# Kernel optimization log

Measured on AMD Instinct MI355X. Metric: run time of the kernel, lower is better.

## Reference

```python
import jax, jax.numpy as jnp
import numpy as np

# Canonical Mamba hyperparams (mamba_ssm defaults for d_model=128)
D_MODEL = 128
D_INNER = 2 * D_MODEL          # expand = 2
D_STATE = 16
D_CONV = 4
DT_RANK = (D_MODEL + 15) // 16  # ceil(d_model/16) = 8
B, N, T = 16, 256, 64
EPS = 1e-5


def setup_inputs() -> dict:
    key = jax.random.key(0)
    ks = jax.random.split(key, 10)
    sc = 0.02
    x = jax.random.normal(ks[0], (B, N, D_MODEL, T), jnp.float32)
    gamma = jnp.ones((D_MODEL,), jnp.float32)
    beta = jnp.zeros((D_MODEL,), jnp.float32)
    W_in = jax.random.normal(ks[1], (D_MODEL, 2 * D_INNER), jnp.float32) * sc
    conv_w = jax.random.normal(ks[2], (D_INNER, D_CONV), jnp.float32) * sc
    conv_b = jnp.zeros((D_INNER,), jnp.float32)
    W_x = jax.random.normal(ks[3], (D_INNER, DT_RANK + 2 * D_STATE), jnp.float32) * sc
    W_dt = jax.random.normal(ks[4], (DT_RANK, D_INNER), jnp.float32) * sc
    b_dt = jax.random.normal(ks[5], (D_INNER,), jnp.float32) * sc
    # S4D-real init: A_log = log(1..d_state), broadcast over channels
    A_log = jnp.log(jnp.broadcast_to(
        jnp.arange(1, D_STATE + 1, dtype=jnp.float32), (D_INNER, D_STATE)))
    Dskip = jnp.ones((D_INNER,), jnp.float32)
    W_out = jax.random.normal(ks[6], (D_INNER, D_MODEL), jnp.float32) * sc
    return dict(x=x, gamma=gamma, beta=beta, W_in=W_in, conv_w=conv_w,
                conv_b=conv_b, W_x=W_x, W_dt=W_dt, b_dt=b_dt,
                A_log=A_log, Dskip=Dskip, W_out=W_out)


def _forward(x, gamma, beta, W_in, conv_w, conv_b, W_x, W_dt, b_dt,
             A_log, Dskip, W_out):
    Bb, Nn, Fd, Tt = x.shape
    # (B,N,F,T) -> (B*N, T, F)
    x_in = x.transpose(0, 1, 3, 2).reshape(Bb * Nn, Tt, Fd)

    # LayerNorm over feature dim
    mu = x_in.mean(-1, keepdims=True)
    var = jnp.mean((x_in - mu) ** 2, axis=-1, keepdims=True)
    u = (x_in - mu) * jax.lax.rsqrt(var + EPS) * gamma + beta

    # Mamba: input projection -> (x, z)
    xz = u @ W_in                                   # (BN,T,2*dI)
    xc, z = jnp.split(xz, 2, axis=-1)

    # Depthwise causal conv1d over time (kernel D_CONV) + SiLU
    xp = jnp.pad(xc, ((0, 0), (D_CONV - 1, 0), (0, 0)))
    xconv = sum(xp[:, k:k + Tt, :] * conv_w[:, k] for k in range(D_CONV)) + conv_b
    xact = jax.nn.silu(xconv)                       # (BN,T,dI)

    # Input-dependent SSM parameters
    dbl = xact @ W_x                                # (BN,T,dt_rank+2*dS)
    dt = dbl[..., :DT_RANK]
    Bm = dbl[..., DT_RANK:DT_RANK + D_STATE]        # (BN,T,dS)
    Cm = dbl[..., DT_RANK + D_STATE:]               # (BN,T,dS)
    delta = jax.nn.softplus(dt @ W_dt + b_dt)       # (BN,T,dI)
    A = -jnp.exp(A_log)                             # (dI,dS)

    # Selective scan over time
    def step(h, inp):
        d, b, c, xt = inp                            # (BN,dI) (BN,dS) (BN,dS) (BN,dI)
        dA = jnp.exp(d[:, :, None] * A)              # (BN,dI,dS)
        h = dA * h + (d * xt)[:, :, None] * b[:, None, :]
        y = jnp.einsum('bis,bs->bi', h, c)
        return h, y

    h0 = jnp.zeros((Bb * Nn, D_INNER, D_STATE), x.dtype)
    seq = (delta.transpose(1, 0, 2), Bm.transpose(1, 0, 2),
           Cm.transpose(1, 0, 2), xact.transpose(1, 0, 2))
    _, ys = jax.lax.scan(step, h0, seq)             # (T,BN,dI)
    y = ys.transpose(1, 0, 2) + xact * Dskip
    y = y * jax.nn.silu(z)
    out = y @ W_out                                 # (BN,T,d_model)

    # Residual (dropout is identity in eval/reference), reshape back
    x_out = out + x_in
    return x_out.reshape(Bb, Nn, Tt, Fd).transpose(0, 1, 3, 2)


def reference(x, gamma, beta, W_in, conv_w, conv_b, W_x, W_dt, b_dt,
              A_log, Dskip, W_out):
    return _forward(x, gamma, beta, W_in, conv_w, conv_b, W_x, W_dt, b_dt,
                    A_log, Dskip, W_out)
```

## Files before the change

kernel.cpp:

```cpp
#include <hip/hip_runtime.h>
#include <stdint.h>

typedef unsigned short ushort_t;
typedef __attribute__((ext_vector_type(8))) short bf16x8;
typedef __attribute__((ext_vector_type(4))) float f32x4;

#define P_CONVW 0
#define P_CONVB 1024
#define P_BDT   1280
#define P_A     1536
#define P_DSKIP 5632
#define P_GAMMA 5888
#define P_BETA  6016
#define P_WDT   6144
#define P_TOT   8192

#define OFFB_WINT   0
#define OFFB_WXT    131072
#define OFFB_WOUTT  163840
#define OFFB_PF     229376
#define OFFB_DYN    262144

__device__ __forceinline__ float b2f(ushort_t u) {
    return __uint_as_float(((unsigned int)u) << 16);
}
__device__ __forceinline__ ushort_t f2b(float f) {
    unsigned int x = __float_as_uint(f);
    return (ushort_t)((x + 0x7fffu + ((x >> 16) & 1u)) >> 16);
}
__device__ __forceinline__ bool is_f32_mode(const void* gamma) {
    return ((const unsigned int*)gamma)[0] == 0x3F800000u;
}
__device__ __forceinline__ float ld_any(const void* p, int idx, bool f32m) {
    return f32m ? ((const float*)p)[idx] : b2f(((const ushort_t*)p)[idx]);
}
__device__ __forceinline__ float silu_f(float v) {
    return v * __builtin_amdgcn_rcpf(1.0f + __expf(-v));
}

__global__ __launch_bounds__(256) void prep_kernel(
    const void* __restrict__ gamma, const void* __restrict__ beta,
    const void* __restrict__ W_in,  const void* __restrict__ conv_w,
    const void* __restrict__ conv_b,const void* __restrict__ W_x,
    const void* __restrict__ W_dt,  const void* __restrict__ b_dt,
    const void* __restrict__ A_log, const void* __restrict__ Dskip,
    const void* __restrict__ W_out, char* __restrict__ wsb)
{
    const bool f32m = is_f32_mode(gamma);
    ushort_t* WinT  = (ushort_t*)(wsb + OFFB_WINT);
    ushort_t* WxT   = (ushort_t*)(wsb + OFFB_WXT);
    ushort_t* WoutT = (ushort_t*)(wsb + OFFB_WOUTT);
    float*    pf    = (float*)(wsb + OFFB_PF);
    int idx = blockIdx.x * 256 + threadIdx.x;

    if (idx < 65536) {
        int n = idx >> 7, k = idx & 127;
        WinT[idx] = f2b(ld_any(W_in, k * 512 + n, f32m));
    }
    if (idx < 16384) {
        int n = idx >> 8, k = idx & 255;
        WxT[idx] = (n < 40) ? f2b(ld_any(W_x, k * 40 + n, f32m)) : (ushort_t)0;
    }
    if (idx < 32768) {
        int n = idx >> 8, k = idx & 255;
        WoutT[idx] = f2b(ld_any(W_out, k * 128 + n, f32m));
    }
    if (idx < 1024) pf[P_CONVW + idx] = ld_any(conv_w, idx, f32m);
    if (idx < 4096) pf[P_A + idx]     = -__expf(ld_any(A_log, idx, f32m));
    if (idx < 2048) pf[P_WDT + idx]   = ld_any(W_dt, idx, f32m);
    if (idx < 256) {
        pf[P_CONVB + idx] = ld_any(conv_b, idx, f32m);
        pf[P_BDT + idx]   = ld_any(b_dt, idx, f32m);
        pf[P_DSKIP + idx] = ld_any(Dskip, idx, f32m);
    }
    if (idx < 128) {
        pf[P_GAMMA + idx] = ld_any(gamma, idx, f32m);
        pf[P_BETA + idx]  = ld_any(beta, idx, f32m);
    }
}

__global__ __launch_bounds__(256) void k_ln(
    const void* __restrict__ x_v, const void* __restrict__ gamma_v,
    const float* __restrict__ pf, ushort_t* __restrict__ u_out, int seq_base)
{
    __shared__ __align__(16) float uT[128 * 72];
    __shared__ float red1[256], red2[256];
    __shared__ float mu_s[64], rs_s[64];

    const int tid = threadIdx.x;
    const int sloc = blockIdx.x;
    const bool f32m = is_f32_mode(gamma_v);
    const size_t seq_off = (size_t)(seq_base + sloc) * (128 * 64);

    {
        int f = tid >> 1, th = tid & 1;
        float* dst = uT + f * 72 + th * 32;
        if (!f32m) {
            const uint4* src = (const uint4*)((const ushort_t*)x_v + seq_off + f * 64 + th * 32);
            #pragma unroll
            for (int i = 0; i < 4; ++i) {
                uint4 q = src[i];
                *(float4*)(dst + i * 8) = make_float4(
                    __uint_as_float(q.x << 16), __uint_as_float(q.x & 0xffff0000u),
                    __uint_as_float(q.y << 16), __uint_as_float(q.y & 0xffff0000u));
                *(float4*)(dst + i * 8 + 4) = make_float4(
                    __uint_as_float(q.z << 16), __uint_as_float(q.z & 0xffff0000u),
                    __uint_as_float(q.w << 16), __uint_as_float(q.w & 0xffff0000u));
            }
        } else {
            const float4* src = (const float4*)((const float*)x_v + seq_off + f * 64 + th * 32);
            #pragma unroll
            for (int i = 0; i < 8; ++i) *(float4*)(dst + i * 4) = src[i];
        }
    }
    __syncthreads();
    {
        int q = tid >> 6, t = tid & 63;
        float su = 0.f, sq = 0.f;
        #pragma unroll 8
        for (int kk = 0; kk < 32; ++kk) {
            float v = uT[(q * 32 + kk) * 72 + t];
            su += v; sq += v * v;
        }
        red1[tid] = su; red2[tid] = sq;
    }
    __syncthreads();
    if (tid < 64) {
        float su = red1[tid] + red1[64 + tid] + red1[128 + tid] + red1[192 + tid];
        float sq = red2[tid] + red2[64 + tid] + red2[128 + tid] + red2[192 + tid];
        float mu = su * (1.0f / 128.0f);
        float var = sq * (1.0f / 128.0f) - mu * mu;
        mu_s[tid] = mu;
        rs_s[tid] = rsqrtf(var + 1e-5f);
    }
    __syncthreads();
    {
        int t = tid & 63, dq = tid >> 6;
        float mu = mu_s[t], rs = rs_s[t];
        unsigned int pk[16];
        #pragma unroll
        for (int j = 0; j < 16; ++j) {
            int d0 = dq * 32 + 2 * j;
            float v0 = (uT[d0 * 72 + t] - mu) * rs * pf[P_GAMMA + d0] + pf[P_BETA + d0];
            float v1 = (uT[(d0 + 1) * 72 + t] - mu) * rs * pf[P_GAMMA + d0 + 1] + pf[P_BETA + d0 + 1];
            pk[j] = (unsigned int)f2b(v0) | ((unsigned int)f2b(v1) << 16);
        }
        uint4* dst = (uint4*)(u_out + (size_t)(sloc * 64 + t) * 128 + dq * 32);
        dst[0] = make_uint4(pk[0], pk[1], pk[2], pk[3]);
        dst[1] = make_uint4(pk[4], pk[5], pk[6], pk[7]);
        dst[2] = make_uint4(pk[8], pk[9], pk[10], pk[11]);
        dst[3] = make_uint4(pk[12], pk[13], pk[14], pk[15]);
    }
}

__global__ __launch_bounds__(512) void k_gemm1(
    const ushort_t* __restrict__ u, const ushort_t* __restrict__ WinT,
    ushort_t* __restrict__ xz, int nrows)
{
    __shared__ __align__(16) ushort_t Afr[16384];
    const int tid = threadIdx.x;
    const int m0 = blockIdx.x * 128;

    #pragma unroll
    for (int i = 0; i < 4; ++i) {
        int g = tid * 4 + i;
        int R = g >> 4, cc = g & 15;
        uint4 val = make_uint4(0u, 0u, 0u, 0u);
        int row = m0 + R;
        if (row < nrows) val = *(const uint4*)(u + (size_t)row * 128 + cc * 8);
        int kstep = cc >> 2, q = cc & 3, mf = R >> 4, r = R & 15;
        *(uint4*)(Afr + (((kstep * 8 + mf) * 64) + q * 16 + r) * 8) = val;
    }
    __syncthreads();

    const int lane = tid & 63, w = tid >> 6;
    const int wm = w & 1, wn = w >> 1;
    const int r = lane & 15, q = lane >> 4;

    #pragma unroll 1
    for (int nt = 0; nt < 4; ++nt) {
        f32x4 acc[4][2];
        #pragma unroll
        for (int i = 0; i < 4; ++i)
            #pragma unroll
            for (int nf = 0; nf < 2; ++nf) acc[i][nf] = (f32x4)(0.0f);

        #pragma unroll
        for (int ks = 0; ks < 4; ++ks) {
            bf16x8 a[4], b[2];
            #pragma unroll
            for (int i = 0; i < 4; ++i)
                a[i] = *(const bf16x8*)(Afr + ((ks * 8 + wm * 4 + i) * 64 + lane) * 8);
            #pragma unroll
            for (int nf = 0; nf < 2; ++nf) {
                int n = nt * 128 + wn * 32 + nf * 16 + r;
                b[nf] = *(const bf16x8*)(WinT + n * 128 + ks * 32 + q * 8);
            }
            #pragma unroll
            for (int i = 0; i < 4; ++i)
                #pragma unroll
                for (int nf = 0; nf < 2; ++nf)
                    acc[i][nf] = __builtin_amdgcn_mfma_f32_16x16x32_bf16(a[i], b[nf], acc[i][nf], 0, 0, 0);
        }
        #pragma unroll
        for (int i = 0; i < 4; ++i)
            #pragma unroll
            for (int nf = 0; nf < 2; ++nf)
                #pragma unroll
                for (int rg = 0; rg < 4; ++rg) {
                    int m = m0 + wm * 64 + i * 16 + q * 4 + rg;
                    if (m < nrows) {
                        int n = nt * 128 + wn * 32 + nf * 16 + r;
                        xz[(size_t)m * 512 + n] = f2b(acc[i][nf][rg]);
                    }
                }
    }
}

__global__ __launch_bounds__(256) void k_fuse(
    const void* __restrict__ x_v, const void* __restrict__ gamma_v,
    const ushort_t* __restrict__ xz, const float* __restrict__ pf,
    const ushort_t* __restrict__ WxT, const ushort_t* __restrict__ WoutT,
    void* __restrict__ out_v, int seq_base)
{
    __shared__ __align__(16) char smem[33792 + 18432];
    ushort_t* xact_s = (ushort_t*)smem;
    float*    dbl_s  = (float*)(smem + 33792);
    ushort_t* outT_s = (ushort_t*)(smem + 33792);

    const int tid = threadIdx.x;
    const int sloc = blockIdx.x;
    const int sglob = seq_base + sloc;
    const bool f32m = is_f32_mode(gamma_v);
    const int lane = tid & 63, w = tid >> 6;
    const int r = lane & 15, q = lane >> 4;

    {
        const int c = tid;
        float cw0 = pf[P_CONVW + c * 4 + 0], cw1 = pf[P_CONVW + c * 4 + 1];
        float cw2 = pf[P_CONVW + c * 4 + 2], cw3 = pf[P_CONVW + c * 4 + 3];
        float cb  = pf[P_CONVB + c];
        float w0 = 0.f, w1 = 0.f, w2 = 0.f;
        const ushort_t* xc = xz + (size_t)sloc * 64 * 512 + c;
        #pragma unroll 4
        for (int t = 0; t < 64; ++t) {
            float xv = b2f(xc[t * 512]);
            float v = cb + w0 * cw0 + w1 * cw1 + w2 * cw2 + xv * cw3;
            xact_s[t * 264 + c] = f2b(silu_f(v));
            w0 = w1; w1 = w2; w2 = xv;
        }
    }
    __syncthreads();

    {
        f32x4 acc2[4];
        #pragma unroll
        for (int i = 0; i < 4; ++i) acc2[i] = (f32x4)(0.0f);
        #pragma unroll 1
        for (int ks = 0; ks < 8; ++ks) {
            bf16x8 b = *(const bf16x8*)(WxT + (w * 16 + r) * 256 + ks * 32 + q * 8);
            #pragma unroll
            for (int i = 0; i < 4; ++i) {
                bf16x8 a = *(const bf16x8*)(xact_s + (i * 16 + r) * 264 + ks * 32 + q * 8);
                acc2[i] = __builtin_amdgcn_mfma_f32_16x16x32_bf16(a, b, acc2[i], 0, 0, 0);
            }
        }
        int col = w * 16 + r;
        if (col < 40) {
            #pragma unroll
            for (int i = 0; i < 4; ++i)
                #pragma unroll
                for (int rg = 0; rg < 4; ++rg)
                    dbl_s[(i * 16 + q * 4 + rg) * 44 + col] = acc2[i][rg];
        }
    }
    __syncthreads();

    {
        const int i = tid;
        float wdt[8];
        #pragma unroll
        for (int rr = 0; rr < 8; ++rr) wdt[rr] = pf[P_WDT + rr * 256 + i];
        float bdt = pf[P_BDT + i];
        float dsk = pf[P_DSKIP + i];
        float Av[16];
        #pragma unroll
        for (int qq = 0; qq < 4; ++qq) {
            float4 a = *(const float4*)(pf + P_A + i * 16 + qq * 4);
            Av[qq*4+0] = a.x; Av[qq*4+1] = a.y; Av[qq*4+2] = a.z; Av[qq*4+3] = a.w;
        }
        float h[16];
        #pragma unroll
        for (int ss = 0; ss < 16; ++ss) h[ss] = 0.f;
        const ushort_t* zc = xz + (size_t)sloc * 64 * 512 + 256 + i;

        #pragma unroll 1
        for (int t = 0; t < 64; ++t) {
            const float* dr = dbl_s + t * 44;
            float4 d0 = *(const float4*)(dr);
            float4 d1 = *(const float4*)(dr + 4);
            float arg = bdt;
            arg = fmaf(d0.x, wdt[0], arg); arg = fmaf(d0.y, wdt[1], arg);
            arg = fmaf(d0.z, wdt[2], arg); arg = fmaf(d0.w, wdt[3], arg);
            arg = fmaf(d1.x, wdt[4], arg); arg = fmaf(d1.y, wdt[5], arg);
            arg = fmaf(d1.z, wdt[6], arg); arg = fmaf(d1.w, wdt[7], arg);
            float delta = __logf(1.0f + __expf(arg));

            float Bv[16], Cv[16];
            #pragma unroll
            for (int qq = 0; qq < 4; ++qq) {
                float4 b = *(const float4*)(dr + 8 + qq * 4);
                Bv[qq*4+0] = b.x; Bv[qq*4+1] = b.y; Bv[qq*4+2] = b.z; Bv[qq*4+3] = b.w;
            }
            #pragma unroll
            for (int qq = 0; qq < 4; ++qq) {
                float4 c = *(const float4*)(dr + 24 + qq * 4);
                Cv[qq*4+0] = c.x; Cv[qq*4+1] = c.y; Cv[qq*4+2] = c.z; Cv[qq*4+3] = c.w;
            }
            float xt = b2f(xact_s[t * 264 + i]);
            float zf = b2f(zc[t * 512]);
            float dx = delta * xt;
            float y = 0.f;
            #pragma unroll
            for (int ss = 0; ss < 16; ++ss) {
                float dA = __expf(delta * Av[ss]);
                h[ss] = fmaf(dA, h[ss], dx * Bv[ss]);
                y = fmaf(h[ss], Cv[ss], y);
            }
            float yg = fmaf(xt, dsk, y) * silu_f(zf);
            xact_s[t * 264 + i] = f2b(yg);
        }
    }
    __syncthreads();

    {
        f32x4 acc3[4][2];
        #pragma unroll
        for (int i = 0; i < 4; ++i)
            #pragma unroll
            for (int nf = 0; nf < 2; ++nf) acc3[i][nf] = (f32x4)(0.0f);
        #pragma unroll 1
        for (int ks = 0; ks < 8; ++ks) {
            bf16x8 a[4], b[2];
            #pragma unroll
            for (int i = 0; i < 4; ++i)
                a[i] = *(const bf16x8*)(xact_s + (i * 16 + r) * 264 + ks * 32 + q * 8);
            #pragma unroll
            for (int nf = 0; nf < 2; ++nf)
                b[nf] = *(const bf16x8*)(WoutT + (w * 32 + nf * 16 + r) * 256 + ks * 32 + q * 8);
            #pragma unroll
            for (int i = 0; i < 4; ++i)
                #pragma unroll
                for (int nf = 0; nf < 2; ++nf)
                    acc3[i][nf] = __builtin_amdgcn_mfma_f32_16x16x32_bf16(a[i], b[nf], acc3[i][nf], 0, 0, 0);
        }
        __syncthreads();
        #pragma unroll
        for (int i = 0; i < 4; ++i)
            #pragma unroll
            for (int nf = 0; nf < 2; ++nf)
                #pragma unroll
                for (int rg = 0; rg < 4; ++rg) {
                    int d = w * 32 + nf * 16 + r;
                    int t = i * 16 + q * 4 + rg;
                    outT_s[d * 72 + t] = f2b(acc3[i][nf][rg]);
                }
    }
    __syncthreads();

    {
        int d2 = tid >> 1, hf = tid & 1;
        const ushort_t* src = outT_s + d2 * 72 + hf * 32;
        if (!f32m) {
            const ushort_t* xr = (const ushort_t*)x_v + (size_t)sglob * 8192 + d2 * 64 + hf * 32;
            ushort_t* ob = (ushort_t*)out_v + (size_t)sglob * 8192 + d2 * 64 + hf * 32;
            #pragma unroll
            for (int cch = 0; cch < 4; ++cch) {
                uint4 ov = *(const uint4*)(src + cch * 8);
                uint4 xv = *(const uint4*)(xr + cch * 8);
                unsigned int* op = (unsigned int*)&ov;
                unsigned int* xp = (unsigned int*)&xv;
                uint4 res;
                unsigned int* rp = (unsigned int*)&res;
                #pragma unroll
                for (int j = 0; j < 4; ++j) {
                    float a0 = __uint_as_float(op[j] << 16) + __uint_as_float(xp[j] << 16);
                    float a1 = __uint_as_float(op[j] & 0xffff0000u) + __uint_as_float(xp[j] & 0xffff0000u);
                    rp[j] = (unsigned int)f2b(a0) | ((unsigned int)f2b(a1) << 16);
                }
                *(uint4*)(ob + cch * 8) = res;
            }
        } else {
            const float* xr = (const float*)x_v + (size_t)sglob * 8192 + d2 * 64 + hf * 32;
            float* ob = (float*)out_v + (size_t)sglob * 8192 + d2 * 64 + hf * 32;
            #pragma unroll
            for (int j = 0; j < 32; ++j)
                ob[j] = b2f(src[j]) + xr[j];
        }
    }
}

extern "C" void kernel_launch(void* const* d_in, const int* in_sizes, int n_in,
                              void* d_out, int out_size, void* d_ws, size_t ws_size,
                              hipStream_t stream)
{
    const void* x      = d_in[0];
    const void* gamma  = d_in[1];
    const void* beta   = d_in[2];
    const void* W_in   = d_in[3];
    const void* conv_w = d_in[4];
    const void* conv_b = d_in[5];
    const void* W_x    = d_in[6];
    const void* W_dt   = d_in[7];
    const void* b_dt   = d_in[8];
    const void* A_log  = d_in[9];
    const void* Dskip  = d_in[10];
    const void* W_out  = d_in[11];

    char* wsb = (char*)d_ws;
    long long avail = (long long)ws_size - OFFB_DYN;
    long long S = avail > 0 ? avail / 81920 : 1;
    if (S > 4096) S = 4096;
    if (S < 1) S = 1;

    ushort_t* WinT  = (ushort_t*)(wsb + OFFB_WINT);
    ushort_t* WxT   = (ushort_t*)(wsb + OFFB_WXT);
    ushort_t* WoutT = (ushort_t*)(wsb + OFFB_WOUTT);
    float*    pf    = (float*)(wsb + OFFB_PF);
    ushort_t* u_buf = (ushort_t*)(wsb + OFFB_DYN);
    ushort_t* xz_buf= (ushort_t*)(wsb + OFFB_DYN + S * 16384);

    prep_kernel<<<dim3(256), dim3(256), 0, stream>>>(
        gamma, beta, W_in, conv_w, conv_b, W_x, W_dt, b_dt, A_log, Dskip, W_out, wsb);

    for (int base = 0; base < 4096; base += (int)S) {
        int cnt = 4096 - base < (int)S ? 4096 - base : (int)S;
        k_ln<<<dim3(cnt), dim3(256), 0, stream>>>(x, gamma, pf, u_buf, base);
        k_gemm1<<<dim3((cnt + 1) / 2), dim3(512), 0, stream>>>(u_buf, WinT, xz_buf, cnt * 64);
        k_fuse<<<dim3(cnt), dim3(256), 0, stream>>>(x, gamma, xz_buf, pf, WxT, WoutT, d_out, base);
    }
}
```

Measured before the change: 718.8 us.

## Replace per-state exp in selective scan with powers of one reciprocal

At runtime the fused kernel checks whether A equals -(s+1), the S4D-real init. If it does, exp(delta*A_s) becomes e1^(s+1) with e1 = 1/(1+exp(arg)), so the 16 exps per step turn into one reciprocal plus repeated multiplies. The scan loop is also software-pipelined to prefetch the next step's operands. B/C are stored in LDS as bf16 to shrink shared memory, and launch bounds now request 4 blocks per CU. The epilogue writes the residual output straight from MFMA accumulators instead of transposing through LDS; the trade-offs are precision loss on B/C and a general fallback path kept for other A values.

```diff
diff --git a/kernel.cpp b/kernel.cpp
--- a/kernel.cpp
+++ b/kernel.cpp
@@ -217,16 +217,16 @@
     }
 }
 
-__global__ __launch_bounds__(256) void k_fuse(
+__global__ __launch_bounds__(256, 4) void k_fuse(
     const void* __restrict__ x_v, const void* __restrict__ gamma_v,
     const ushort_t* __restrict__ xz, const float* __restrict__ pf,
     const ushort_t* __restrict__ WxT, const ushort_t* __restrict__ WoutT,
     void* __restrict__ out_v, int seq_base)
 {
-    __shared__ __align__(16) char smem[33792 + 18432];
+    __shared__ __align__(16) char smem[40448];
     ushort_t* xact_s = (ushort_t*)smem;
-    float*    dbl_s  = (float*)(smem + 33792);
-    ushort_t* outT_s = (ushort_t*)(smem + 33792);
+    float*    dt_s   = (float*)(smem + 33792);
+    ushort_t* BC_s   = (ushort_t*)(smem + 35840);
 
     const int tid = threadIdx.x;
     const int sloc = blockIdx.x;
@@ -266,13 +266,15 @@
             }
         }
         int col = w * 16 + r;
-        if (col < 40) {
-            #pragma unroll
-            for (int i = 0; i < 4; ++i)
-                #pragma unroll
-                for (int rg = 0; rg < 4; ++rg)
-                    dbl_s[(i * 16 + q * 4 + rg) * 44 + col] = acc2[i][rg];
-        }
+        #pragma unroll
+        for (int i = 0; i < 4; ++i)
+            #pragma unroll
+            for (int rg = 0; rg < 4; ++rg) {
+                int trow = i * 16 + q * 4 + rg;
+                float v = acc2[i][rg];
+                if (col < 8)       dt_s[trow * 8 + col] = v;
+                else if (col < 40) BC_s[trow * 36 + (col - 8)] = f2b(v);
+            }
     }
     __syncthreads();
 
@@ -281,54 +283,150 @@
         float wdt[8];
         #pragma unroll
         for (int rr = 0; rr < 8; ++rr) wdt[rr] = pf[P_WDT + rr * 256 + i];
-        float bdt = pf[P_BDT + i];
-        float dsk = pf[P_DSKIP + i];
-        float Av[16];
-        #pragma unroll
-        for (int qq = 0; qq < 4; ++qq) {
-            float4 a = *(const float4*)(pf + P_A + i * 16 + qq * 4);
-            Av[qq*4+0] = a.x; Av[qq*4+1] = a.y; Av[qq*4+2] = a.z; Av[qq*4+3] = a.w;
-        }
+        const float bdt = pf[P_BDT + i];
+        const float dsk = pf[P_DSKIP + i];
+
+        bool structured = true;
+        #pragma unroll
+        for (int ss = 0; ss < 16; ++ss) {
+            float av = pf[P_A + i * 16 + ss];
+            structured = structured && (fabsf(av + (float)(ss + 1)) <= 1e-3f * (float)(ss + 1));
+        }
+
         float h[16];
         #pragma unroll
         for (int ss = 0; ss < 16; ++ss) h[ss] = 0.f;
         const ushort_t* zc = xz + (size_t)sloc * 64 * 512 + 256 + i;
 
-        #pragma unroll 1
-        for (int t = 0; t < 64; ++t) {
-            const float* dr = dbl_s + t * 44;
-            float4 d0 = *(const float4*)(dr);
+        auto dt_arg = [&](int t) -> float {
+            const float* dr = dt_s + t * 8;
+            float4 d0 = *(const float4*)dr;
             float4 d1 = *(const float4*)(dr + 4);
             float arg = bdt;
             arg = fmaf(d0.x, wdt[0], arg); arg = fmaf(d0.y, wdt[1], arg);
             arg = fmaf(d0.z, wdt[2], arg); arg = fmaf(d0.w, wdt[3], arg);
             arg = fmaf(d1.x, wdt[4], arg); arg = fmaf(d1.y, wdt[5], arg);
             arg = fmaf(d1.z, wdt[6], arg); arg = fmaf(d1.w, wdt[7], arg);
-            float delta = __logf(1.0f + __expf(arg));
-
-            float Bv[16], Cv[16];
-            #pragma unroll
-            for (int qq = 0; qq < 4; ++qq) {
-                float4 b = *(const float4*)(dr + 8 + qq * 4);
-                Bv[qq*4+0] = b.x; Bv[qq*4+1] = b.y; Bv[qq*4+2] = b.z; Bv[qq*4+3] = b.w;
-            }
-            #pragma unroll
-            for (int qq = 0; qq < 4; ++qq) {
-                float4 c = *(const float4*)(dr + 24 + qq * 4);
-                Cv[qq*4+0] = c.x; Cv[qq*4+1] = c.y; Cv[qq*4+2] = c.z; Cv[qq*4+3] = c.w;
-            }
-            float xt = b2f(xact_s[t * 264 + i]);
-            float zf = b2f(zc[t * 512]);
-            float dx = delta * xt;
-            float y = 0.f;
-            #pragma unroll
-            for (int ss = 0; ss < 16; ++ss) {
-                float dA = __expf(delta * Av[ss]);
-                h[ss] = fmaf(dA, h[ss], dx * Bv[ss]);
-                y = fmaf(h[ss], Cv[ss], y);
-            }
-            float yg = fmaf(xt, dsk, y) * silu_f(zf);
-            xact_s[t * 264 + i] = f2b(yg);
+            return arg;
+        };
+
+        if (structured) {
+            auto scan_step = [&](int t, float delv, float e1v, float xtv,
+                                 ushort_t zv, const unsigned int* pk) {
+                float Bv[16], Cv[16];
+                #pragma unroll
+                for (int jj = 0; jj < 8; ++jj) {
+                    unsigned int v = pk[jj];
+                    Bv[2 * jj]     = __uint_as_float(v << 16);
+                    Bv[2 * jj + 1] = __uint_as_float(v & 0xffff0000u);
+                }
+                #pragma unroll
+                for (int jj = 0; jj < 8; ++jj) {
+                    unsigned int v = pk[8 + jj];
+                    Cv[2 * jj]     = __uint_as_float(v << 16);
+                    Cv[2 * jj + 1] = __uint_as_float(v & 0xffff0000u);
+                }
+                float dx = delv * xtv;
+                float dA = e1v;
+                float yp[4] = {0.f, 0.f, 0.f, 0.f};
+                #pragma unroll
+                for (int ss = 0; ss < 16; ++ss) {
+                    h[ss] = fmaf(dA, h[ss], dx * Bv[ss]);
+                    yp[ss & 3] = fmaf(h[ss], Cv[ss], yp[ss & 3]);
+                    dA *= e1v;
+                }
+                float y = (yp[0] + yp[1]) + (yp[2] + yp[3]);
+                float yg = fmaf(xtv, dsk, y) * silu_f(b2f(zv));
+                xact_s[t * 264 + i] = f2b(yg);
+            };
+
+            float e1_c, del_c;
+            {
+                float arg = dt_arg(0);
+                float p = __expf(arg);
+                float opp = 1.0f + p;
+                e1_c = __builtin_amdgcn_rcpf(opp);
+                del_c = __logf(opp);
+            }
+            unsigned int pk_c[16];
+            {
+                const uint2* bq = (const uint2*)(BC_s);
+                #pragma unroll
+                for (int jj = 0; jj < 8; ++jj) {
+                    uint2 vv = bq[jj];
+                    pk_c[2 * jj] = vv.x; pk_c[2 * jj + 1] = vv.y;
+                }
+            }
+            float xt_c = b2f(xact_s[i]);
+            ushort_t z_c = zc[0];
+            ushort_t z_n = zc[512];
+
+            #pragma unroll 1
+            for (int t = 0; t < 63; ++t) {
+                float arg = dt_arg(t + 1);
+                float p = __expf(arg);
+                float opp = 1.0f + p;
+                float e1_n = __builtin_amdgcn_rcpf(opp);
+                float del_n = __logf(opp);
+                unsigned int pk_n[16];
+                {
+                    const uint2* bq = (const uint2*)(BC_s + (t + 1) * 36);
+                    #pragma unroll
+                    for (int jj = 0; jj < 8; ++jj) {
+                        uint2 vv = bq[jj];
+                        pk_n[2 * jj] = vv.x; pk_n[2 * jj + 1] = vv.y;
+                    }
+                }
+                float xt_n = b2f(xact_s[(t + 1) * 264 + i]);
+                int tz = (t + 2 <= 63) ? (t + 2) : 63;
+                ushort_t z_n2 = zc[(size_t)tz * 512];
+
+                scan_step(t, del_c, e1_c, xt_c, z_c, pk_c);
+
+                e1_c = e1_n; del_c = del_n; xt_c = xt_n;
+                z_c = z_n; z_n = z_n2;
+                #pragma unroll
+                for (int jj = 0; jj < 16; ++jj) pk_c[jj] = pk_n[jj];
+            }
+            scan_step(63, del_c, e1_c, xt_c, z_c, pk_c);
+        } else {
+            float Av[16];
+            #pragma unroll
+            for (int ss = 0; ss < 16; ++ss) Av[ss] = pf[P_A + i * 16 + ss];
+            #pragma unroll 1
+            for (int t = 0; t < 64; ++t) {
+                float arg = dt_arg(t);
+                float delta = __logf(1.0f + __expf(arg));
+                unsigned int pk[16];
+                const uint2* bq = (const uint2*)(BC_s + t * 36);
+                #pragma unroll
+                for (int jj = 0; jj < 8; ++jj) {
+                    uint2 vv = bq[jj];
+                    pk[2 * jj] = vv.x; pk[2 * jj + 1] = vv.y;
+                }
+                float Bv[16], Cv[16];
+                #pragma unroll
+                for (int jj = 0; jj < 8; ++jj) {
+                    unsigned int v = pk[jj];
+                    Bv[2 * jj]     = __uint_as_float(v << 16);
+                    Bv[2 * jj + 1] = __uint_as_float(v & 0xffff0000u);
+                    unsigned int vc = pk[8 + jj];
+                    Cv[2 * jj]     = __uint_as_float(vc << 16);
+                    Cv[2 * jj + 1] = __uint_as_float(vc & 0xffff0000u);
+                }
+                float xt = b2f(xact_s[t * 264 + i]);
+                float zf = b2f(zc[t * 512]);
+                float dx = delta * xt;
+                float y = 0.f;
+                #pragma unroll
+                for (int ss = 0; ss < 16; ++ss) {
+                    float dA = __expf(delta * Av[ss]);
+                    h[ss] = fmaf(dA, h[ss], dx * Bv[ss]);
+                    y = fmaf(h[ss], Cv[ss], y);
+                }
+                float yg = fmaf(xt, dsk, y) * silu_f(zf);
+                xact_s[t * 264 + i] = f2b(yg);
+            }
         }
     }
     __syncthreads();
@@ -354,48 +452,41 @@
                 for (int nf = 0; nf < 2; ++nf)
                     acc3[i][nf] = __builtin_amdgcn_mfma_f32_16x16x32_bf16(a[i], b[nf], acc3[i][nf], 0, 0, 0);
         }
-        __syncthreads();
-        #pragma unroll
-        for (int i = 0; i < 4; ++i)
-            #pragma unroll
-            for (int nf = 0; nf < 2; ++nf)
-                #pragma unroll
-                for (int rg = 0; rg < 4; ++rg) {
+        if (!f32m) {
+            #pragma unroll
+            for (int i = 0; i < 4; ++i)
+                #pragma unroll
+                for (int nf = 0; nf < 2; ++nf) {
                     int d = w * 32 + nf * 16 + r;
-                    int t = i * 16 + q * 4 + rg;
-                    outT_s[d * 72 + t] = f2b(acc3[i][nf][rg]);
-                }
-    }
-    __syncthreads();
-
-    {
-        int d2 = tid >> 1, hf = tid & 1;
-        const ushort_t* src = outT_s + d2 * 72 + hf * 32;
-        if (!f32m) {
-            const ushort_t* xr = (const ushort_t*)x_v + (size_t)sglob * 8192 + d2 * 64 + hf * 32;
-            ushort_t* ob = (ushort_t*)out_v + (size_t)sglob * 8192 + d2 * 64 + hf * 32;
-            #pragma unroll
-            for (int cch = 0; cch < 4; ++cch) {
-                uint4 ov = *(const uint4*)(src + cch * 8);
-                uint4 xv = *(const uint4*)(xr + cch * 8);
-                unsigned int* op = (unsigned int*)&ov;
-                unsigned int* xp = (unsigned int*)&xv;
-                uint4 res;
-                unsigned int* rp = (unsigned int*)&res;
-                #pragma unroll
-                for (int j = 0; j < 4; ++j) {
-                    float a0 = __uint_as_float(op[j] << 16) + __uint_as_float(xp[j] << 16);
-                    float a1 = __uint_as_float(op[j] & 0xffff0000u) + __uint_as_float(xp[j] & 0xffff0000u);
-                    rp[j] = (unsigned int)f2b(a0) | ((unsigned int)f2b(a1) << 16);
-                }
-                *(uint4*)(ob + cch * 8) = res;
-            }
+                    int tb = i * 16 + q * 4;
+                    size_t off = (size_t)sglob * 8192 + (size_t)d * 64 + tb;
+                    uint2 xv = *(const uint2*)((const ushort_t*)x_v + off);
+                    float x0 = __uint_as_float(xv.x << 16);
+                    float x1 = __uint_as_float(xv.x & 0xffff0000u);
+                    float x2 = __uint_as_float(xv.y << 16);
+                    float x3 = __uint_as_float(xv.y & 0xffff0000u);
+                    uint2 res;
+                    res.x = (unsigned int)f2b(acc3[i][nf][0] + x0) |
+                            ((unsigned int)f2b(acc3[i][nf][1] + x1) << 16);
+                    res.y = (unsigned int)f2b(acc3[i][nf][2] + x2) |
+                            ((unsigned int)f2b(acc3[i][nf][3] + x3) << 16);
+                    *(uint2*)((ushort_t*)out_v + off) = res;
+                }
         } else {
-            const float* xr = (const float*)x_v + (size_t)sglob * 8192 + d2 * 64 + hf * 32;
-            float* ob = (float*)out_v + (size_t)sglob * 8192 + d2 * 64 + hf * 32;
-            #pragma unroll
-            for (int j = 0; j < 32; ++j)
-                ob[j] = b2f(src[j]) + xr[j];
+            #pragma unroll
+            for (int i = 0; i < 4; ++i)
+                #pragma unroll
+                for (int nf = 0; nf < 2; ++nf) {
+                    int d = w * 32 + nf * 16 + r;
+                    int tb = i * 16 + q * 4;
+                    size_t off = (size_t)sglob * 8192 + (size_t)d * 64 + tb;
+                    float4 xv = *(const float4*)((const float*)x_v + off);
+                    float4 res = make_float4(acc3[i][nf][0] + xv.x,
+                                             acc3[i][nf][1] + xv.y,
+                                             acc3[i][nf][2] + xv.z,
+                                             acc3[i][nf][3] + xv.w);
+                    *(float4*)((float*)out_v + off) = res;
+                }
         }
     }
 }
```

After: 691.5 us. 1.04x faster.
